# Optimization experiments

Hardware: AMD Instinct MI355X
Metric: run time of the kernel (lower is better)

The kernel has to match this reference:

```python
import jax, jax.numpy as jnp
import numpy as np

GAMMA = 2.0
ASPECT_W = 1.0
OPINION_W = 1.0
SENTIMENT_W = 1.0
BOUNDARY_W = 0.5
IGNORE = -100

B, S, C_SPAN, C_SENT = 256, 8192, 3, 3


def setup_inputs() -> dict:
    key = jax.random.key(0)
    k1, k2, k3, k4, k5, k6, k7 = jax.random.split(key, 7)
    return {
        "aspect_logits": jax.random.normal(k1, (B, S, C_SPAN), dtype=jnp.float32),
        "opinion_logits": jax.random.normal(k2, (B, S, C_SPAN), dtype=jnp.float32),
        "sentiment_logits": jax.random.normal(k3, (B, C_SENT), dtype=jnp.float32),
        "boundary_logits": jax.random.normal(k4, (B, S, 2), dtype=jnp.float32),
        "aspect_labels": jax.random.randint(k5, (B, S), 0, 3, dtype=jnp.int32),
        "opinion_labels": jax.random.randint(k6, (B, S), 0, 3, dtype=jnp.int32),
        "sentiment_labels": jax.random.randint(k7, (B,), 0, 3, dtype=jnp.int32),
    }


def _masked_ce(logits2d, labels1d):
    """Per-position CE with ignore_index=-100; returns (ce, valid_mask)."""
    valid = labels1d != IGNORE
    safe = jnp.where(valid, labels1d, 0)
    logp = jax.nn.log_softmax(logits2d, axis=-1)
    ce = -jnp.take_along_axis(logp, safe[:, None], axis=-1)[:, 0]
    ce = jnp.where(valid, ce, 0.0)
    return ce, valid


def _focal_loss(logits, labels, gamma):
    C = logits.shape[-1]
    ce, valid = _masked_ce(logits.reshape(-1, C), labels.reshape(-1))
    pt = jnp.exp(-ce)
    fl = (1.0 - pt) ** gamma * ce
    n = valid.sum().astype(fl.dtype)
    return jnp.where(n > 0, fl.sum() / jnp.maximum(n, 1.0), 0.0)


def _boundary_labels(span_labels):
    """Vectorized version of the per-batch Python-loop boundary construction.
    start: label==1; end: label==2 and next label != 2 (last pos counts if ==2)."""
    start = (span_labels == 1)
    nxt = jnp.concatenate(
        [span_labels[:, 1:], jnp.full_like(span_labels[:, :1], -1)], axis=1)
    end = (span_labels == 2) & (nxt != 2)
    return start, end


def reference(aspect_logits, opinion_logits, sentiment_logits, boundary_logits,
              aspect_labels, opinion_labels, sentiment_labels):
    # focal span losses
    aspect_loss = _focal_loss(aspect_logits, aspect_labels, GAMMA)
    opinion_loss = _focal_loss(opinion_logits, opinion_labels, GAMMA)

    # sentiment CE (mean over valid)
    ce_s, valid_s = _masked_ce(sentiment_logits, sentiment_labels)
    n_s = valid_s.sum().astype(ce_s.dtype)
    sentiment_loss = ce_s.sum() / jnp.maximum(n_s, 1.0)

    # boundary labels: OR of aspect/opinion starts and ends
    a_start, a_end = _boundary_labels(aspect_labels)
    o_start, o_end = _boundary_labels(opinion_labels)
    start = (a_start | o_start).astype(boundary_logits.dtype)
    end = (a_end | o_end).astype(boundary_logits.dtype)
    y = jnp.stack([start, end], axis=-1)  # [B, S, 2]

    z = boundary_logits
    bce = jnp.maximum(z, 0.0) - z * y + jnp.log1p(jnp.exp(-jnp.abs(z)))
    boundary_loss = bce.mean()

    total = (ASPECT_W * aspect_loss + OPINION_W * opinion_loss +
             SENTIMENT_W * sentiment_loss + BOUNDARY_W * boundary_loss)
    return total
```

## Files before the change

### kernel.cpp

```cpp
#include <hip/hip_runtime.h>

constexpr int BB = 256;
constexpr int SS = 8192;
constexpr int NPOS = BB * SS;
constexpr int IGNORE = -100;
constexpr int BLOCKS = NPOS / 4 / 256;

__device__ __forceinline__ void focal_acc(float l0, float l1, float l2,
                                          int lab, float& fl, float& cnt) {
    if (lab == IGNORE) return;
    float m   = fmaxf(l0, fmaxf(l1, l2));
    float s   = __expf(l0 - m) + __expf(l1 - m) + __expf(l2 - m);
    float lse = m + __logf(s);
    float x   = (lab == 0) ? l0 : ((lab == 1) ? l1 : l2);
    float ce  = lse - x;
    float pt  = __expf(-ce);
    float om  = 1.0f - pt;
    fl  += om * om * ce;
    cnt += 1.0f;
}

__device__ __forceinline__ float bce_term(float z, float y) {
    return fmaxf(z, 0.0f) - z * y + __logf(1.0f + __expf(-fabsf(z)));
}

__global__ __launch_bounds__(256)
void main_kernel(const float* __restrict__ a_logits,
                 const float* __restrict__ o_logits,
                 const float* __restrict__ b_logits,
                 const int*   __restrict__ a_labels,
                 const int*   __restrict__ o_labels,
                 float*       __restrict__ partial) {
    int t = blockIdx.x * blockDim.x + threadIdx.x;
    float fl_a = 0.f, cnt_a = 0.f, fl_o = 0.f, cnt_o = 0.f, bce = 0.f;

    {
        int p0 = t * 4;
        int lane = threadIdx.x & 63;

        int4 al4 = *(const int4*)(a_labels + p0);
        int4 ol4 = *(const int4*)(o_labels + p0);

        int al_next = __shfl_down(al4.x, 1, 64);
        int ol_next = __shfl_down(ol4.x, 1, 64);
        if (lane == 63) {
            if (((p0 + 3) & (SS - 1)) != SS - 1) {
                al_next = a_labels[p0 + 4];
                ol_next = o_labels[p0 + 4];
            } else {
                al_next = -1;
                ol_next = -1;
            }
        }
        int al[5] = {al4.x, al4.y, al4.z, al4.w, al_next};
        int ol[5] = {ol4.x, ol4.y, ol4.z, ol4.w, ol_next};

        const float4* ap = (const float4*)(a_logits + p0 * 3);
        const float4* op = (const float4*)(o_logits + p0 * 3);
        float4 A0 = ap[0], A1 = ap[1], A2 = ap[2];
        float4 O0 = op[0], O1 = op[1], O2 = op[2];
        float aL[12] = {A0.x, A0.y, A0.z, A0.w, A1.x, A1.y, A1.z, A1.w,
                        A2.x, A2.y, A2.z, A2.w};
        float oL[12] = {O0.x, O0.y, O0.z, O0.w, O1.x, O1.y, O1.z, O1.w,
                        O2.x, O2.y, O2.z, O2.w};

        const float4* bp = (const float4*)(b_logits + p0 * 2);
        float4 Z0 = bp[0], Z1 = bp[1];
        float z[8] = {Z0.x, Z0.y, Z0.z, Z0.w, Z1.x, Z1.y, Z1.z, Z1.w};

        #pragma unroll
        for (int j = 0; j < 4; ++j) {
            focal_acc(aL[3*j], aL[3*j+1], aL[3*j+2], al[j], fl_a, cnt_a);
            focal_acc(oL[3*j], oL[3*j+1], oL[3*j+2], ol[j], fl_o, cnt_o);
            float ys = ((al[j] == 1) || (ol[j] == 1)) ? 1.0f : 0.0f;
            float ye = (((al[j] == 2) && (al[j+1] != 2)) ||
                        ((ol[j] == 2) && (ol[j+1] != 2))) ? 1.0f : 0.0f;
            bce += bce_term(z[2*j],     ys);
            bce += bce_term(z[2*j + 1], ye);
        }
    }

    float vals[5] = {fl_a, cnt_a, fl_o, cnt_o, bce};
    #pragma unroll
    for (int k = 0; k < 5; ++k) {
        float v = vals[k];
        #pragma unroll
        for (int o = 32; o > 0; o >>= 1) v += __shfl_down(v, o, 64);
        vals[k] = v;
    }
    __shared__ float lds[4 * 5];
    int lane = threadIdx.x & 63, wid = threadIdx.x >> 6;
    if (lane == 0) {
        #pragma unroll
        for (int k = 0; k < 5; ++k) lds[wid * 5 + k] = vals[k];
    }
    __syncthreads();
    if (threadIdx.x == 0) {
        #pragma unroll
        for (int k = 0; k < 5; ++k) {
            float s = lds[k] + lds[5 + k] + lds[10 + k] + lds[15 + k];
            partial[k * BLOCKS + blockIdx.x] = s;
        }
    }
}

__global__ __launch_bounds__(256)
void sent_final_kernel(const float* __restrict__ s_logits,
                       const int*   __restrict__ s_labels,
                       const float* __restrict__ partial,
                       float* __restrict__ out) {
    int tid = threadIdx.x;

    float acc[5];
    #pragma unroll
    for (int k = 0; k < 5; ++k) {
        float s = 0.f;
        #pragma unroll
        for (int i = 0; i < BLOCKS / 256; ++i)
            s += partial[k * BLOCKS + tid + i * 256];
        acc[k] = s;
    }

    float ce = 0.f, cnt = 0.f;
    {
        int lab = s_labels[tid];
        if (lab != IGNORE) {
            float l0 = s_logits[3*tid], l1 = s_logits[3*tid+1], l2 = s_logits[3*tid+2];
            float m   = fmaxf(l0, fmaxf(l1, l2));
            float lse = m + __logf(__expf(l0-m) + __expf(l1-m) + __expf(l2-m));
            float x   = (lab == 0) ? l0 : ((lab == 1) ? l1 : l2);
            ce  = lse - x;
            cnt = 1.0f;
        }
    }

    float vals[7] = {acc[0], acc[1], acc[2], acc[3], acc[4], ce, cnt};
    #pragma unroll
    for (int k = 0; k < 7; ++k) {
        float v = vals[k];
        #pragma unroll
        for (int o = 32; o > 0; o >>= 1) v += __shfl_down(v, o, 64);
        vals[k] = v;
    }
    __shared__ float lds[4 * 7];
    int lane = threadIdx.x & 63, wid = threadIdx.x >> 6;
    if (lane == 0) {
        #pragma unroll
        for (int k = 0; k < 7; ++k) lds[wid * 7 + k] = vals[k];
    }
    __syncthreads();
    if (threadIdx.x == 0) {
        float tot[7];
        #pragma unroll
        for (int k = 0; k < 7; ++k)
            tot[k] = lds[k] + lds[7 + k] + lds[14 + k] + lds[21 + k];
        double fl_a = tot[0], ca = tot[1], fl_o = tot[2], co = tot[3];
        double bsum = tot[4], sv = tot[5], sc = tot[6];
        double aspect  = (ca > 0.0) ? fl_a / fmax(ca, 1.0) : 0.0;
        double opinion = (co > 0.0) ? fl_o / fmax(co, 1.0) : 0.0;
        double senti   = sv / fmax(sc, 1.0);
        double bnd     = bsum / (double)((long long)NPOS * 2);
        out[0] = (float)(aspect + opinion + senti + 0.5 * bnd);
    }
}

extern "C" void kernel_launch(void* const* d_in, const int* in_sizes, int n_in,
                              void* d_out, int out_size, void* d_ws, size_t ws_size,
                              hipStream_t stream) {
    const float* a_logits = (const float*)d_in[0];
    const float* o_logits = (const float*)d_in[1];
    const float* s_logits = (const float*)d_in[2];
    const float* b_logits = (const float*)d_in[3];
    const int*   a_labels = (const int*)d_in[4];
    const int*   o_labels = (const int*)d_in[5];
    const int*   s_labels = (const int*)d_in[6];
    float* out = (float*)d_out;
    float* partial = (float*)d_ws;

    main_kernel<<<BLOCKS, 256, 0, stream>>>(a_logits, o_logits, b_logits,
                                            a_labels, o_labels, partial);
    sent_final_kernel<<<1, 256, 0, stream>>>(s_logits, s_labels, partial, out);
}
```

Before: 115.4 us.

## Fuse final reduction into main kernel via last-block atomic ticket; cheaper focal pt

Merges the separate single-block finalize kernel into the main kernel: each block publishes its partials and takes an atomic ticket, and the last block to finish performs the final reduction and sentiment CE. The counter is zeroed with a memset on the stream, so the second kernel launch is replaced by a memset node. It also computes pt from the already-computed exponent times a reciprocal instead of a separate exp. This aims to remove launch gaps and some transcendental work, at the cost of an atomic per block and a memset.

```diff
diff --git a/kernel.cpp b/kernel.cpp
--- a/kernel.cpp
+++ b/kernel.cpp
@@ -5,17 +5,19 @@
 constexpr int NPOS = BB * SS;
 constexpr int IGNORE = -100;
 constexpr int BLOCKS = NPOS / 4 / 256;
+constexpr int CTR_OFF_FLOATS = 5 * BLOCKS;
 
 __device__ __forceinline__ void focal_acc(float l0, float l1, float l2,
                                           int lab, float& fl, float& cnt) {
     if (lab == IGNORE) return;
-    float m   = fmaxf(l0, fmaxf(l1, l2));
-    float s   = __expf(l0 - m) + __expf(l1 - m) + __expf(l2 - m);
-    float lse = m + __logf(s);
-    float x   = (lab == 0) ? l0 : ((lab == 1) ? l1 : l2);
-    float ce  = lse - x;
-    float pt  = __expf(-ce);
-    float om  = 1.0f - pt;
+    float m  = fmaxf(l0, fmaxf(l1, l2));
+    float e0 = __expf(l0 - m), e1 = __expf(l1 - m), e2 = __expf(l2 - m);
+    float s  = e0 + e1 + e2;
+    float x  = (lab == 0) ? l0 : ((lab == 1) ? l1 : l2);
+    float el = (lab == 0) ? e0 : ((lab == 1) ? e1 : e2);
+    float ce = __logf(s) + (m - x);
+    float pt = el * __builtin_amdgcn_rcpf(s);
+    float om = 1.0f - pt;
     fl  += om * om * ce;
     cnt += 1.0f;
 }
@@ -25,17 +27,21 @@
 }
 
 __global__ __launch_bounds__(256)
-void main_kernel(const float* __restrict__ a_logits,
-                 const float* __restrict__ o_logits,
-                 const float* __restrict__ b_logits,
-                 const int*   __restrict__ a_labels,
-                 const int*   __restrict__ o_labels,
-                 float*       __restrict__ partial) {
+void fused_kernel(const float* __restrict__ a_logits,
+                  const float* __restrict__ o_logits,
+                  const float* __restrict__ b_logits,
+                  const float* __restrict__ s_logits,
+                  const int*   __restrict__ a_labels,
+                  const int*   __restrict__ o_labels,
+                  const int*   __restrict__ s_labels,
+                  float*       __restrict__ partial,
+                  unsigned*    __restrict__ counter,
+                  float*       __restrict__ out) {
     int t = blockIdx.x * blockDim.x + threadIdx.x;
     float fl_a = 0.f, cnt_a = 0.f, fl_o = 0.f, cnt_o = 0.f, bce = 0.f;
 
     {
-        int p0 = t * 4;
+        int p0   = t * 4;
         int lane = threadIdx.x & 63;
 
         int4 al4 = *(const int4*)(a_labels + p0);
@@ -88,27 +94,27 @@
         for (int o = 32; o > 0; o >>= 1) v += __shfl_down(v, o, 64);
         vals[k] = v;
     }
-    __shared__ float lds[4 * 5];
+    __shared__ float lds5[4 * 5];
+    __shared__ unsigned ticket;
     int lane = threadIdx.x & 63, wid = threadIdx.x >> 6;
     if (lane == 0) {
         #pragma unroll
-        for (int k = 0; k < 5; ++k) lds[wid * 5 + k] = vals[k];
+        for (int k = 0; k < 5; ++k) lds5[wid * 5 + k] = vals[k];
     }
     __syncthreads();
     if (threadIdx.x == 0) {
         #pragma unroll
         for (int k = 0; k < 5; ++k) {
-            float s = lds[k] + lds[5 + k] + lds[10 + k] + lds[15 + k];
-            partial[k * BLOCKS + blockIdx.x] = s;
+            float s = lds5[k] + lds5[5 + k] + lds5[10 + k] + lds5[15 + k];
+            __hip_atomic_store(&partial[k * BLOCKS + blockIdx.x], s,
+                               __ATOMIC_RELAXED, __HIP_MEMORY_SCOPE_AGENT);
         }
+        ticket = __hip_atomic_fetch_add(counter, 1u, __ATOMIC_ACQ_REL,
+                                        __HIP_MEMORY_SCOPE_AGENT);
     }
-}
+    __syncthreads();
+    if (ticket != (unsigned)(BLOCKS - 1)) return;
 
-__global__ __launch_bounds__(256)
-void sent_final_kernel(const float* __restrict__ s_logits,
-                       const int*   __restrict__ s_labels,
-                       const float* __restrict__ partial,
-                       float* __restrict__ out) {
     int tid = threadIdx.x;
 
     float acc[5];
@@ -117,7 +123,8 @@
         float s = 0.f;
         #pragma unroll
         for (int i = 0; i < BLOCKS / 256; ++i)
-            s += partial[k * BLOCKS + tid + i * 256];
+            s += __hip_atomic_load(&partial[k * BLOCKS + tid + i * 256],
+                                   __ATOMIC_RELAXED, __HIP_MEMORY_SCOPE_AGENT);
         acc[k] = s;
     }
 
@@ -134,26 +141,25 @@
         }
     }
 
-    float vals[7] = {acc[0], acc[1], acc[2], acc[3], acc[4], ce, cnt};
+    float fv[7] = {acc[0], acc[1], acc[2], acc[3], acc[4], ce, cnt};
     #pragma unroll
     for (int k = 0; k < 7; ++k) {
-        float v = vals[k];
+        float v = fv[k];
         #pragma unroll
         for (int o = 32; o > 0; o >>= 1) v += __shfl_down(v, o, 64);
-        vals[k] = v;
+        fv[k] = v;
     }
-    __shared__ float lds[4 * 7];
-    int lane = threadIdx.x & 63, wid = threadIdx.x >> 6;
+    __shared__ float lds7[4 * 7];
     if (lane == 0) {
         #pragma unroll
-        for (int k = 0; k < 7; ++k) lds[wid * 7 + k] = vals[k];
+        for (int k = 0; k < 7; ++k) lds7[wid * 7 + k] = fv[k];
     }
     __syncthreads();
-    if (threadIdx.x == 0) {
+    if (tid == 0) {
         float tot[7];
         #pragma unroll
         for (int k = 0; k < 7; ++k)
-            tot[k] = lds[k] + lds[7 + k] + lds[14 + k] + lds[21 + k];
+            tot[k] = lds7[k] + lds7[7 + k] + lds7[14 + k] + lds7[21 + k];
         double fl_a = tot[0], ca = tot[1], fl_o = tot[2], co = tot[3];
         double bsum = tot[4], sv = tot[5], sc = tot[6];
         double aspect  = (ca > 0.0) ? fl_a / fmax(ca, 1.0) : 0.0;
@@ -174,10 +180,13 @@
     const int*   a_labels = (const int*)d_in[4];
     const int*   o_labels = (const int*)d_in[5];
     const int*   s_labels = (const int*)d_in[6];
-    float* out = (float*)d_out;
+    float* out     = (float*)d_out;
     float* partial = (float*)d_ws;
+    unsigned* counter = (unsigned*)((char*)d_ws + CTR_OFF_FLOATS * sizeof(float));
 
-    main_kernel<<<BLOCKS, 256, 0, stream>>>(a_logits, o_logits, b_logits,
-                                            a_labels, o_labels, partial);
-    sent_final_kernel<<<1, 256, 0, stream>>>(s_logits, s_labels, partial, out);
+    hipMemsetAsync(counter, 0, sizeof(unsigned), stream);
+
+    fused_kernel<<<BLOCKS, 256, 0, stream>>>(a_logits, o_logits, b_logits,
+                                             s_logits, a_labels, o_labels,
+                                             s_labels, partial, counter, out);
 }
```

Measured after the change: 197.9 us. 71.5% more time.
